# Performance work log

Measured on AMD Instinct MI355X. Metric: run time of the kernel, lower is better.

The kernel has to match this reference:

```python
import jax, jax.numpy as jnp
import numpy as np

IGNORE = 5
N_CLASS = 5
MAX_VIEWS = 2048
MAX_VIEWS_BG = 4096


def setup_inputs() -> dict:
    key = jax.random.key(0)
    ks = jax.random.split(key, 8)
    B, C, H, W = 8, 512, 128, 128
    HF, WF = 1024, 1024
    feats = jax.random.normal(ks[0], (B, C, H, W), dtype=jnp.float32)
    labels = jax.random.uniform(ks[1], (B, HF, WF, N_CLASS), dtype=jnp.float32)
    predicts = jax.random.randint(ks[2], (B, H, W), 0, N_CLASS).astype(jnp.int32)
    s = 0.02
    w1 = jax.random.normal(ks[3], (512, 512), jnp.float32) * s
    b1 = jnp.zeros((512,), jnp.float32)
    w2 = jax.random.normal(ks[4], (256, 512), jnp.float32) * s
    b2 = jnp.zeros((256,), jnp.float32)
    w3 = jax.random.normal(ks[5], (256, 256), jnp.float32) * s
    b3 = jnp.zeros((256,), jnp.float32)
    return dict(feats=feats, labels=labels, predicts=predicts,
                w1=w1, b1=b1, w2=w2, b2=b2, w3=w3, b3=b3)


def _leaky(x):
    return jnp.where(x >= 0, x, 0.2 * x)


def _proj_head(x, w1, b1, w2, b2, w3, b3):
    # Linear -> LeakyReLU(0.2) -> Linear -> LeakyReLU(0.2) -> Linear, then L2-normalize (dim=1)
    h = _leaky(x @ w1.T + b1)
    h = _leaky(h @ w2.T + b2)
    h = h @ w3.T + b3
    nrm = jnp.maximum(jnp.linalg.norm(h, axis=1, keepdims=True), 1e-12)
    return h / nrm


def _sample_class(y_hat, y, feats0, c, mv):
    """Stratified hard/easy pixel selection for class c, padded to static size mv.
    Deterministic take-first-k replaces torch.randperm for reproducibility."""
    N = y_hat.shape[0]
    hard = (y_hat == c) & (y != c)
    easy = (y_hat == c) & (y == c)
    nh = hard.sum().astype(jnp.int32)
    ne = easy.sum().astype(jnp.int32)
    cnt = nh + ne
    valid = (cnt > 1).astype(jnp.int32)   # classes with <=1 pixel are skipped in the original
    n_sel = jnp.minimum(cnt, mv) * valid
    both = (2 * nh >= n_sel) & (2 * ne >= n_sel)
    hk = jnp.where(both, n_sel // 2,
                   jnp.where(2 * nh >= n_sel, n_sel - ne, nh))
    ek = n_sel - hk
    idx = jnp.arange(N, dtype=jnp.int32)
    hsel = hard & ((jnp.cumsum(hard) - 1) < hk)   # first hk hard pixels
    esel = easy & ((jnp.cumsum(easy) - 1) < ek)   # first ek easy pixels
    # stream-compaction: hard first, then easy, then padding
    sort_key = jnp.where(hsel, idx, jnp.where(esel, idx + N, 2 * N))
    order = jnp.argsort(sort_key)[:mv]            # static slice of size mv
    row_ok = jnp.arange(mv) < n_sel
    X = feats0[order] * row_ok[:, None]           # zero-pad invalid rows
    yc = jnp.where(row_ok, c, IGNORE)
    return X, yc.astype(jnp.int32)


def reference(feats, labels, predicts, w1, b1, w2, b2, w3, b3):
    B, C, H, W = feats.shape
    lab = jnp.argmax(labels, axis=-1)             # [B, HF, WF]
    sh, sw = lab.shape[1] // H, lab.shape[2] // W
    lab_ds = lab[:, ::sh, ::sw]                   # nearest-neighbor downsample (integer factor)
    # original _hard_anchor_sampling returns inside the batch loop -> only image 0 contributes
    y_hat = lab_ds[0].reshape(-1).astype(jnp.int32)
    y = predicts[0].reshape(-1).astype(jnp.int32)
    feats0 = feats[0].transpose(1, 2, 0).reshape(H * W, C)  # NHWC flatten
    Xs, ys = [], []
    for c in range(N_CLASS):                      # static small class loop
        mv = MAX_VIEWS_BG if c == 0 else MAX_VIEWS
        Xc, yc = _sample_class(y_hat, y, feats0, c, mv)
        Xs.append(Xc)
        ys.append(yc)
    X_ = jnp.concatenate(Xs, axis=0)              # [MV_bg + 4*MV, 512]
    y_ = jnp.concatenate(ys, axis=0)
    anchors = _proj_head(X_, w1, b1, w2, b2, w3, b3)
    return anchors, y_
```

## Files before the change

kernel.cpp:

```cpp
#include <hip/hip_runtime.h>

#define HW 16384
#define IGN 5
#define ROWS_TOTAL 12288
#define ANCH_ELEMS (ROWS_TOTAL * 256)

typedef __bf16 bf16x8 __attribute__((ext_vector_type(8)));
typedef float f32x4 __attribute__((ext_vector_type(4)));
typedef unsigned long long ull;

#define GLDS16(g, l)                                                                     \
    __builtin_amdgcn_global_load_lds((__attribute__((address_space(1))) const void*)(g), \
                                     (__attribute__((address_space(3))) void*)(l), 16, 0, 0)

__device__ __forceinline__ int swz_off(int row, int chunk) {
    return row * 64 + ((chunk ^ (row & 7)) * 8);
}

__global__ void prep_kernel(const float* __restrict__ labels, const int* __restrict__ predicts,
                            int* __restrict__ y_hat, ull* __restrict__ maskH,
                            ull* __restrict__ maskE, int* __restrict__ fwd) {
    int p = blockIdx.x * 256 + threadIdx.x;
    int pr = p >> 7, pc = p & 127;
    const float* lp = labels + ((size_t)(pr * 8) * 1024 + (size_t)(pc * 8)) * 5;
    float best = lp[0];
    int bi = 0;
#pragma unroll
    for (int c = 1; c < 5; ++c) {
        float v = lp[c];
        if (v > best) { best = v; bi = c; }
    }
    y_hat[p] = bi;
    if (p < ROWS_TOTAL) fwd[p] = -1;
    int yy = predicts[p];
    int chunk = p >> 6;
    int lane = threadIdx.x & 63;
#pragma unroll
    for (int c = 0; c < 5; ++c) {
        ull mh = __ballot(bi == c && yy != c);
        ull me = __ballot(bi == c && yy == c);
        if (lane == 0) {
            maskH[c * 256 + chunk] = mh;
            maskE[c * 256 + chunk] = me;
        }
    }
}

__global__ void scan_kernel(const ull* __restrict__ maskH, const ull* __restrict__ maskE,
                            int* __restrict__ baseH, int* __restrict__ baseE,
                            int* __restrict__ nsel, int* __restrict__ hkA,
                            int* __restrict__ ekA) {
    int c = threadIdx.x >> 6;
    int lane = threadIdx.x & 63;
    if (c >= 5) return;
    int ph[4], pe[4];
    int sh = 0, se = 0;
#pragma unroll
    for (int k = 0; k < 4; ++k) {
        int ch = lane * 4 + k;
        ph[k] = sh;
        sh += __popcll(maskH[c * 256 + ch]);
        pe[k] = se;
        se += __popcll(maskE[c * 256 + ch]);
    }
    int incH = sh, incE = se;
#pragma unroll
    for (int d = 1; d < 64; d <<= 1) {
        int t = __shfl_up(incH, d);
        if (lane >= d) incH += t;
        t = __shfl_up(incE, d);
        if (lane >= d) incE += t;
    }
    int exH = incH - sh, exE = incE - se;
#pragma unroll
    for (int k = 0; k < 4; ++k) {
        baseH[c * 256 + lane * 4 + k] = exH + ph[k];
        baseE[c * 256 + lane * 4 + k] = exE + pe[k];
    }
    int nh = __shfl(incH, 63), ne = __shfl(incE, 63);
    if (lane == 0) {
        int mv = (c == 0) ? 4096 : 2048;
        int cnt = nh + ne;
        int n_sel = (cnt > 1) ? ((cnt < mv) ? cnt : mv) : 0;
        int hk;
        if ((2 * nh >= n_sel) && (2 * ne >= n_sel)) hk = n_sel >> 1;
        else if (2 * nh >= n_sel) hk = n_sel - ne;
        else hk = nh;
        nsel[c] = n_sel;
        hkA[c] = hk;
        ekA[c] = n_sel - hk;
    }
}

__global__ void write_inv_kernel(const int* __restrict__ y_hat,
                                 const ull* __restrict__ maskH, const ull* __restrict__ maskE,
                                 const int* __restrict__ baseH, const int* __restrict__ baseE,
                                 const int* __restrict__ hkA, const int* __restrict__ ekA,
                                 const int* __restrict__ nsel, int* __restrict__ fwd,
                                 float* __restrict__ out) {
    int p = blockIdx.x * 256 + threadIdx.x;
    int chunk = p >> 6;
    int lane = threadIdx.x & 63;
    int c = y_hat[p];
    ull mh = maskH[c * 256 + chunk];
    ull me = maskE[c * 256 + chunk];
    ull below = (1ull << lane) - 1ull;
    int cls_base = (c == 0) ? 0 : 4096 + (c - 1) * 2048;
    int res = -1;
    if ((mh >> lane) & 1ull) {
        int pos = baseH[c * 256 + chunk] + __popcll(mh & below);
        if (pos < hkA[c]) res = cls_base + pos;
    } else if ((me >> lane) & 1ull) {
        int pos = baseE[c * 256 + chunk] + __popcll(me & below);
        if (pos < ekA[c]) res = cls_base + hkA[c] + pos;
    }
    if (res >= 0) fwd[res] = p;
    if (p < ROWS_TOTAL) {
        int cc, rin;
        if (p < 4096) { cc = 0; rin = p; }
        else { cc = 1 + ((p - 4096) >> 11); rin = (p - 4096) & 2047; }
        out[ANCH_ELEMS + p] = (float)(rin < nsel[cc] ? cc : IGN);
    }
}

__global__ void conv_x_kernel(const float* __restrict__ F, __bf16* __restrict__ Xb) {
    __shared__ float t[32 * 33];
    int pb = blockIdx.x * 32, chb = blockIdx.y * 32;
    int tid = threadIdx.x;
    int il = tid & 31;
    int grp = tid >> 5;
#pragma unroll
    for (int it = 0; it < 4; ++it) {
        int ch = grp + it * 8;
        t[il * 33 + ch] = F[(size_t)(chb + ch) * HW + pb + il];
    }
    __syncthreads();
#pragma unroll
    for (int it = 0; it < 4; ++it) {
        int p = grp + it * 8;
        Xb[(size_t)(pb + p) * 512 + chb + il] = (__bf16)t[p * 33 + il];
    }
}

__global__ void conv_w_kernel(const float* __restrict__ w1, const float* __restrict__ w2,
                              const float* __restrict__ w3, __bf16* __restrict__ w1b,
                              __bf16* __restrict__ w2b, __bf16* __restrict__ w3b) {
    int i = blockIdx.x * 256 + threadIdx.x;
    if (i < 262144) w1b[i] = (__bf16)w1[i];
    else if (i < 393216) w2b[i - 262144] = (__bf16)w2[i - 262144];
    else if (i < 458752) w3b[i - 393216] = (__bf16)w3[i - 393216];
}

__global__ __launch_bounds__(256) void gemm_bt(const __bf16* __restrict__ A,
                                               const int* __restrict__ fwd,
                                               const __bf16* __restrict__ Bw,
                                               const float* __restrict__ bias,
                                               __bf16* __restrict__ C, int N, int K,
                                               int leaky) {
    const int BK = 64;
    __shared__ __bf16 As[64 * 64];
    __shared__ __bf16 Bs[128 * 64];
    int tid = threadIdx.x;
    int lane = tid & 63;
    int wave_base = tid & 0xC0;
    int wave = tid >> 6;
    int wm = (wave >> 1) * 32, wn = (wave & 1) * 64;
    int mb = blockIdx.y * 64, nb = blockIdx.x * 128;
    int l15 = lane & 15, quad = lane >> 4;

    const __bf16* srcA[2];
    const __bf16* srcB[4];
#pragma unroll
    for (int r = 0; r < 2; ++r) {
        int cc = tid + r * 256;
        int row = cc >> 3, ch = cc & 7;
        int g = mb + row;
        int pix = fwd ? fwd[g] : g;
        if (pix < 0) pix = 0;
        srcA[r] = A + (size_t)pix * K + ((ch ^ (row & 7)) * 8);
    }
#pragma unroll
    for (int r = 0; r < 4; ++r) {
        int cc = tid + r * 256;
        int row = cc >> 3, ch = cc & 7;
        srcB[r] = Bw + (size_t)(nb + row) * K + ((ch ^ (row & 7)) * 8);
    }

    f32x4 acc[2][4] = {};

    for (int kt = 0; kt < K; kt += BK) {
#pragma unroll
        for (int r = 0; r < 2; ++r)
            GLDS16(srcA[r] + kt, As + (size_t)(r * 256 + wave_base) * 8);
#pragma unroll
        for (int r = 0; r < 4; ++r)
            GLDS16(srcB[r] + kt, Bs + (size_t)(r * 256 + wave_base) * 8);
        __syncthreads();
#pragma unroll
        for (int kk = 0; kk < 2; ++kk) {
            bf16x8 af[2], bq[4];
#pragma unroll
            for (int i = 0; i < 2; ++i)
                af[i] = *(const bf16x8*)(As + swz_off(wm + i * 16 + l15, quad + kk * 4));
#pragma unroll
            for (int j = 0; j < 4; ++j)
                bq[j] = *(const bf16x8*)(Bs + swz_off(wn + j * 16 + l15, quad + kk * 4));
#pragma unroll
            for (int i = 0; i < 2; ++i)
#pragma unroll
                for (int j = 0; j < 4; ++j)
                    acc[i][j] = __builtin_amdgcn_mfma_f32_16x16x32_bf16(af[i], bq[j], acc[i][j], 0, 0, 0);
        }
        __syncthreads();
    }

#pragma unroll
    for (int i = 0; i < 2; ++i) {
#pragma unroll
        for (int j = 0; j < 4; ++j) {
            int col = nb + wn + j * 16 + l15;
            float bv = bias[col];
#pragma unroll
            for (int r = 0; r < 4; ++r) {
                int row = mb + wm + i * 16 + quad * 4 + r;
                float v = acc[i][j][r] + bv;
                if (leaky) v = (v >= 0.f) ? v : 0.2f * v;
                C[(size_t)row * N + col] = (__bf16)v;
            }
        }
    }
}

__global__ __launch_bounds__(256) void gemm3_norm(const __bf16* __restrict__ A,
                                                  const __bf16* __restrict__ W,
                                                  const float* __restrict__ bias,
                                                  const int* __restrict__ fwd,
                                                  float* __restrict__ out) {
    const int BK = 64, K = 256;
    __shared__ __bf16 As[64 * 64];
    __shared__ __bf16 Bs[256 * 64];
    __shared__ __bf16 lo[64 * 264];
    __shared__ float nrm[64];
    int tid = threadIdx.x;
    int lane = tid & 63, wave = tid >> 6;
    int wave_base = tid & 0xC0;
    int l15 = lane & 15, quad = lane >> 4;
    int mb = blockIdx.x * 64;
    int wn = wave * 64;

    if (tid < 64) nrm[tid] = 0.f;

    const __bf16* srcA[2];
    const __bf16* srcB[8];
#pragma unroll
    for (int r = 0; r < 2; ++r) {
        int cc = tid + r * 256;
        int row = cc >> 3, ch = cc & 7;
        srcA[r] = A + (size_t)(mb + row) * K + ((ch ^ (row & 7)) * 8);
    }
#pragma unroll
    for (int r = 0; r < 8; ++r) {
        int cc = tid + r * 256;
        int row = cc >> 3, ch = cc & 7;
        srcB[r] = W + (size_t)row * K + ((ch ^ (row & 7)) * 8);
    }

    f32x4 acc[4][4] = {};

    for (int kt = 0; kt < K; kt += BK) {
#pragma unroll
        for (int r = 0; r < 2; ++r)
            GLDS16(srcA[r] + kt, As + (size_t)(r * 256 + wave_base) * 8);
#pragma unroll
        for (int r = 0; r < 8; ++r)
            GLDS16(srcB[r] + kt, Bs + (size_t)(r * 256 + wave_base) * 8);
        __syncthreads();
#pragma unroll
        for (int kk = 0; kk < 2; ++kk) {
            bf16x8 af[4], bq[4];
#pragma unroll
            for (int i = 0; i < 4; ++i)
                af[i] = *(const bf16x8*)(As + swz_off(i * 16 + l15, quad + kk * 4));
#pragma unroll
            for (int j = 0; j < 4; ++j)
                bq[j] = *(const bf16x8*)(Bs + swz_off(wn + j * 16 + l15, quad + kk * 4));
#pragma unroll
            for (int i = 0; i < 4; ++i)
#pragma unroll
                for (int j = 0; j < 4; ++j)
                    acc[i][j] = __builtin_amdgcn_mfma_f32_16x16x32_bf16(af[i], bq[j], acc[i][j], 0, 0, 0);
        }
        __syncthreads();
    }

#pragma unroll
    for (int i = 0; i < 4; ++i) {
#pragma unroll
        for (int r = 0; r < 4; ++r) {
            int row = i * 16 + quad * 4 + r;
            float s = 0.f;
#pragma unroll
            for (int j = 0; j < 4; ++j) {
                int col = wn + j * 16 + l15;
                float v = acc[i][j][r] + bias[col];
                lo[row * 264 + col] = (__bf16)v;
                s += v * v;
            }
            atomicAdd(&nrm[row], s);
        }
    }
    __syncthreads();
    if (tid < 64) {
        float f = 1.0f / fmaxf(sqrtf(nrm[tid]), 1e-12f);
        nrm[tid] = (fwd[mb + tid] >= 0) ? f : 0.f;
    }
    __syncthreads();

#pragma unroll 4
    for (int r = 0; r < 64; ++r) {
        out[(size_t)(mb + r) * 256 + tid] = (float)lo[r * 264 + tid] * nrm[r];
    }
}

extern "C" void kernel_launch(void* const* d_in, const int* in_sizes, int n_in,
                              void* d_out, int out_size, void* d_ws, size_t ws_size,
                              hipStream_t stream) {
    const float* feats = (const float*)d_in[0];
    const float* labels = (const float*)d_in[1];
    const int* predicts = (const int*)d_in[2];
    const float* w1 = (const float*)d_in[3];
    const float* b1 = (const float*)d_in[4];
    const float* w2 = (const float*)d_in[5];
    const float* b2 = (const float*)d_in[6];
    const float* w3 = (const float*)d_in[7];
    const float* b3 = (const float*)d_in[8];
    float* out = (float*)d_out;
    char* ws = (char*)d_ws;

    int* y_hat = (int*)(ws + 0);
    int* fwd = (int*)(ws + (64 << 10));
    int* nsel = (int*)(ws + (128 << 10));
    int* hkA = (int*)(ws + (128 << 10) + 64);
    int* ekA = (int*)(ws + (128 << 10) + 128);
    ull* maskH = (ull*)(ws + (136 << 10));
    ull* maskE = (ull*)(ws + (148 << 10));
    int* baseH = (int*)(ws + (160 << 10));
    int* baseE = (int*)(ws + (168 << 10));
    __bf16* w1b = (__bf16*)(ws + (256 << 10));
    __bf16* w2b = (__bf16*)(ws + (768 << 10));
    __bf16* w3b = (__bf16*)(ws + (1024 << 10));
    __bf16* Xb = (__bf16*)(ws + (2ull << 20));
    __bf16* H1 = (__bf16*)(ws + (18ull << 20));
    __bf16* H2 = (__bf16*)(ws + (34ull << 20));

    prep_kernel<<<64, 256, 0, stream>>>(labels, predicts, y_hat, maskH, maskE, fwd);
    scan_kernel<<<1, 320, 0, stream>>>(maskH, maskE, baseH, baseE, nsel, hkA, ekA);
    write_inv_kernel<<<64, 256, 0, stream>>>(y_hat, maskH, maskE, baseH, baseE, hkA, ekA,
                                             nsel, fwd, out);
    conv_x_kernel<<<dim3(512, 16), 256, 0, stream>>>(feats, Xb);
    conv_w_kernel<<<1792, 256, 0, stream>>>(w1, w2, w3, w1b, w2b, w3b);
    gemm_bt<<<dim3(4, 192), 256, 0, stream>>>(Xb, fwd, w1b, b1, H1, 512, 512, 1);
    gemm_bt<<<dim3(2, 192), 256, 0, stream>>>(H1, nullptr, w2b, b2, H2, 256, 512, 1);
    gemm3_norm<<<192, 256, 0, stream>>>(H2, w3b, b3, fwd, out);
}
```

Baseline: 430.8 us.

## Fuse prep/convert kernels and merge GEMM2+GEMM3+normalize into one kernel

Merges label prep, weight conversion and the feature transpose into a single launch, with wider vectorized float4/bf16x8 accesses in the transpose. Fuses the second and third MLP layers plus L2 normalization into one kernel that keeps the H2 tile in LDS, so H2 is never written to global memory. The norm is now reduced with shuffles, and the GEMM1 grid is reordered to iterate M-major. This removes launch overhead and intermediate global traffic. In exchange the fused kernel uses more LDS per block with 32-row tiles, and the W3 load is serialized after GEMM2.

```diff
diff --git a/kernel.cpp b/kernel.cpp
--- a/kernel.cpp
+++ b/kernel.cpp
@@ -17,32 +17,78 @@
     return row * 64 + ((chunk ^ (row & 7)) * 8);
 }
 
-__global__ void prep_kernel(const float* __restrict__ labels, const int* __restrict__ predicts,
-                            int* __restrict__ y_hat, ull* __restrict__ maskH,
-                            ull* __restrict__ maskE, int* __restrict__ fwd) {
-    int p = blockIdx.x * 256 + threadIdx.x;
-    int pr = p >> 7, pc = p & 127;
-    const float* lp = labels + ((size_t)(pr * 8) * 1024 + (size_t)(pc * 8)) * 5;
-    float best = lp[0];
-    int bi = 0;
-#pragma unroll
-    for (int c = 1; c < 5; ++c) {
-        float v = lp[c];
-        if (v > best) { best = v; bi = c; }
-    }
-    y_hat[p] = bi;
-    if (p < ROWS_TOTAL) fwd[p] = -1;
-    int yy = predicts[p];
-    int chunk = p >> 6;
-    int lane = threadIdx.x & 63;
-#pragma unroll
-    for (int c = 0; c < 5; ++c) {
-        ull mh = __ballot(bi == c && yy != c);
-        ull me = __ballot(bi == c && yy == c);
-        if (lane == 0) {
-            maskH[c * 256 + chunk] = mh;
-            maskE[c * 256 + chunk] = me;
-        }
+__global__ void prep_fused(const float* __restrict__ labels, const int* __restrict__ predicts,
+                           int* __restrict__ y_hat, ull* __restrict__ maskH,
+                           ull* __restrict__ maskE, int* __restrict__ fwd,
+                           const float* __restrict__ w1, const float* __restrict__ w2,
+                           const float* __restrict__ w3, __bf16* __restrict__ w1b,
+                           __bf16* __restrict__ w2b, __bf16* __restrict__ w3b,
+                           const float* __restrict__ F, __bf16* __restrict__ Xb) {
+    __shared__ float t[64][68];
+    int bid = blockIdx.x;
+    int tid = threadIdx.x;
+    if (bid < 64) {
+        int p = bid * 256 + tid;
+        int pr = p >> 7, pc = p & 127;
+        const float* lp = labels + ((size_t)(pr * 8) * 1024 + (size_t)(pc * 8)) * 5;
+        float best = lp[0];
+        int bi = 0;
+#pragma unroll
+        for (int c = 1; c < 5; ++c) {
+            float v = lp[c];
+            if (v > best) { best = v; bi = c; }
+        }
+        y_hat[p] = bi;
+        if (p < ROWS_TOTAL) fwd[p] = -1;
+        int yy = predicts[p];
+        int chunk = p >> 6;
+        int lane = tid & 63;
+#pragma unroll
+        for (int c = 0; c < 5; ++c) {
+            ull mh = __ballot(bi == c && yy != c);
+            ull me = __ballot(bi == c && yy == c);
+            if (lane == 0) {
+                maskH[c * 256 + chunk] = mh;
+                maskE[c * 256 + chunk] = me;
+            }
+        }
+    } else if (bid < 512) {
+        int base = ((bid - 64) * 256 + tid) * 4;
+        if (base < 262144) {
+            float4 v = *(const float4*)(w1 + base);
+            w1b[base + 0] = (__bf16)v.x; w1b[base + 1] = (__bf16)v.y;
+            w1b[base + 2] = (__bf16)v.z; w1b[base + 3] = (__bf16)v.w;
+        } else if (base < 393216) {
+            int o = base - 262144;
+            float4 v = *(const float4*)(w2 + o);
+            w2b[o + 0] = (__bf16)v.x; w2b[o + 1] = (__bf16)v.y;
+            w2b[o + 2] = (__bf16)v.z; w2b[o + 3] = (__bf16)v.w;
+        } else {
+            int o = base - 393216;
+            float4 v = *(const float4*)(w3 + o);
+            w3b[o + 0] = (__bf16)v.x; w3b[o + 1] = (__bf16)v.y;
+            w3b[o + 2] = (__bf16)v.z; w3b[o + 3] = (__bf16)v.w;
+        }
+    } else {
+        int cid = bid - 512;
+        int pb = (cid & 255) * 64;
+        int chb = (cid >> 8) * 64;
+        int row = tid >> 2;
+        int seg = tid & 3;
+        const float* src = F + (size_t)(chb + row) * HW + pb + seg * 16;
+#pragma unroll
+        for (int k = 0; k < 4; ++k)
+            *(float4*)&t[row][seg * 16 + k * 4] = *(const float4*)(src + k * 4);
+        __syncthreads();
+        int p = tid >> 2;
+        __bf16* dst = Xb + (size_t)(pb + p) * 512 + chb + seg * 16;
+        bf16x8 o0, o1;
+#pragma unroll
+        for (int j = 0; j < 8; ++j) o0[j] = (__bf16)t[seg * 16 + j][p];
+#pragma unroll
+        for (int j = 0; j < 8; ++j) o1[j] = (__bf16)t[seg * 16 + 8 + j][p];
+        *(bf16x8*)dst = o0;
+        *(bf16x8*)(dst + 8) = o1;
     }
 }
 
@@ -123,34 +169,6 @@
     }
 }
 
-__global__ void conv_x_kernel(const float* __restrict__ F, __bf16* __restrict__ Xb) {
-    __shared__ float t[32 * 33];
-    int pb = blockIdx.x * 32, chb = blockIdx.y * 32;
-    int tid = threadIdx.x;
-    int il = tid & 31;
-    int grp = tid >> 5;
-#pragma unroll
-    for (int it = 0; it < 4; ++it) {
-        int ch = grp + it * 8;
-        t[il * 33 + ch] = F[(size_t)(chb + ch) * HW + pb + il];
-    }
-    __syncthreads();
-#pragma unroll
-    for (int it = 0; it < 4; ++it) {
-        int p = grp + it * 8;
-        Xb[(size_t)(pb + p) * 512 + chb + il] = (__bf16)t[p * 33 + il];
-    }
-}
-
-__global__ void conv_w_kernel(const float* __restrict__ w1, const float* __restrict__ w2,
-                              const float* __restrict__ w3, __bf16* __restrict__ w1b,
-                              __bf16* __restrict__ w2b, __bf16* __restrict__ w3b) {
-    int i = blockIdx.x * 256 + threadIdx.x;
-    if (i < 262144) w1b[i] = (__bf16)w1[i];
-    else if (i < 393216) w2b[i - 262144] = (__bf16)w2[i - 262144];
-    else if (i < 458752) w3b[i - 393216] = (__bf16)w3[i - 393216];
-}
-
 __global__ __launch_bounds__(256) void gemm_bt(const __bf16* __restrict__ A,
                                                const int* __restrict__ fwd,
                                                const __bf16* __restrict__ Bw,
@@ -165,7 +183,7 @@
     int wave_base = tid & 0xC0;
     int wave = tid >> 6;
     int wm = (wave >> 1) * 32, wn = (wave & 1) * 64;
-    int mb = blockIdx.y * 64, nb = blockIdx.x * 128;
+    int mb = blockIdx.x * 64, nb = blockIdx.y * 128;
     int l15 = lane & 15, quad = lane >> 4;
 
     const __bf16* srcA[2];
@@ -231,61 +249,54 @@
     }
 }
 
-__global__ __launch_bounds__(256) void gemm3_norm(const __bf16* __restrict__ A,
-                                                  const __bf16* __restrict__ W,
-                                                  const float* __restrict__ bias,
-                                                  const int* __restrict__ fwd,
-                                                  float* __restrict__ out) {
-    const int BK = 64, K = 256;
-    __shared__ __bf16 As[64 * 64];
-    __shared__ __bf16 Bs[256 * 64];
-    __shared__ __bf16 lo[64 * 264];
-    __shared__ float nrm[64];
+__global__ __launch_bounds__(256) void gemm23_norm(const __bf16* __restrict__ H1,
+                                                   const __bf16* __restrict__ W2b,
+                                                   const float* __restrict__ b2,
+                                                   const __bf16* __restrict__ W3b,
+                                                   const float* __restrict__ b3,
+                                                   const int* __restrict__ fwd,
+                                                   float* __restrict__ out) {
+    __shared__ __bf16 As[32 * 64];
+    __shared__ __bf16 Ws[256 * 64];
+    __shared__ __bf16 H2s[4][32 * 64];
+    __shared__ float nrm[32];
     int tid = threadIdx.x;
     int lane = tid & 63, wave = tid >> 6;
     int wave_base = tid & 0xC0;
     int l15 = lane & 15, quad = lane >> 4;
-    int mb = blockIdx.x * 64;
+    int mb = blockIdx.x * 32;
     int wn = wave * 64;
 
-    if (tid < 64) nrm[tid] = 0.f;
-
-    const __bf16* srcA[2];
-    const __bf16* srcB[8];
-#pragma unroll
-    for (int r = 0; r < 2; ++r) {
-        int cc = tid + r * 256;
-        int row = cc >> 3, ch = cc & 7;
-        srcA[r] = A + (size_t)(mb + row) * K + ((ch ^ (row & 7)) * 8);
-    }
+    if (tid < 32) nrm[tid] = 0.f;
+
+    int rowA = tid >> 3, chA = tid & 7;
+    const __bf16* srcA = H1 + (size_t)(mb + rowA) * 512 + ((chA ^ (rowA & 7)) * 8);
+    const __bf16* srcW2[8];
 #pragma unroll
     for (int r = 0; r < 8; ++r) {
         int cc = tid + r * 256;
         int row = cc >> 3, ch = cc & 7;
-        srcB[r] = W + (size_t)row * K + ((ch ^ (row & 7)) * 8);
-    }
-
-    f32x4 acc[4][4] = {};
-
-    for (int kt = 0; kt < K; kt += BK) {
-#pragma unroll
-        for (int r = 0; r < 2; ++r)
-            GLDS16(srcA[r] + kt, As + (size_t)(r * 256 + wave_base) * 8);
+        srcW2[r] = W2b + (size_t)row * 512 + ((ch ^ (row & 7)) * 8);
+    }
+
+    f32x4 acc[2][4] = {};
+    for (int kt = 0; kt < 512; kt += 64) {
+        GLDS16(srcA + kt, As + (size_t)wave_base * 8);
 #pragma unroll
         for (int r = 0; r < 8; ++r)
-            GLDS16(srcB[r] + kt, Bs + (size_t)(r * 256 + wave_base) * 8);
+            GLDS16(srcW2[r] + kt, Ws + (size_t)(r * 256 + wave_base) * 8);
         __syncthreads();
 #pragma unroll
         for (int kk = 0; kk < 2; ++kk) {
-            bf16x8 af[4], bq[4];
-#pragma unroll
-            for (int i = 0; i < 4; ++i)
+            bf16x8 af[2], bq[4];
+#pragma unroll
+            for (int i = 0; i < 2; ++i)
                 af[i] = *(const bf16x8*)(As + swz_off(i * 16 + l15, quad + kk * 4));
 #pragma unroll
             for (int j = 0; j < 4; ++j)
-                bq[j] = *(const bf16x8*)(Bs + swz_off(wn + j * 16 + l15, quad + kk * 4));
-#pragma unroll
-            for (int i = 0; i < 4; ++i)
+                bq[j] = *(const bf16x8*)(Ws + swz_off(wn + j * 16 + l15, quad + kk * 4));
+#pragma unroll
+            for (int i = 0; i < 2; ++i)
 #pragma unroll
                 for (int j = 0; j < 4; ++j)
                     acc[i][j] = __builtin_amdgcn_mfma_f32_16x16x32_bf16(af[i], bq[j], acc[i][j], 0, 0, 0);
@@ -294,31 +305,104 @@
     }
 
 #pragma unroll
-    for (int i = 0; i < 4; ++i) {
+    for (int i = 0; i < 2; ++i) {
+#pragma unroll
+        for (int j = 0; j < 4; ++j) {
+            int col = wn + j * 16 + l15;
+            float bv = b2[col];
+            int ktb = col >> 6;
+            int chunk = (col >> 3) & 7;
+#pragma unroll
+            for (int r = 0; r < 4; ++r) {
+                int row = i * 16 + quad * 4 + r;
+                float v = acc[i][j][r] + bv;
+                v = (v >= 0.f) ? v : 0.2f * v;
+                H2s[ktb][row * 64 + ((chunk ^ (row & 7)) * 8) + (col & 7)] = (__bf16)v;
+            }
+        }
+    }
+    __syncthreads();
+
+    const __bf16* srcW3[8];
+#pragma unroll
+    for (int r = 0; r < 8; ++r) {
+        int cc = tid + r * 256;
+        int row = cc >> 3, ch = cc & 7;
+        srcW3[r] = W3b + (size_t)row * 256 + ((ch ^ (row & 7)) * 8);
+    }
+    f32x4 acc3[2][4] = {};
+    for (int ktb = 0; ktb < 4; ++ktb) {
+#pragma unroll
+        for (int r = 0; r < 8; ++r)
+            GLDS16(srcW3[r] + ktb * 64, Ws + (size_t)(r * 256 + wave_base) * 8);
+        __syncthreads();
+#pragma unroll
+        for (int kk = 0; kk < 2; ++kk) {
+            bf16x8 af[2], bq[4];
+#pragma unroll
+            for (int i = 0; i < 2; ++i)
+                af[i] = *(const bf16x8*)(&H2s[ktb][0] + swz_off(i * 16 + l15, quad + kk * 4));
+#pragma unroll
+            for (int j = 0; j < 4; ++j)
+                bq[j] = *(const bf16x8*)(Ws + swz_off(wn + j * 16 + l15, quad + kk * 4));
+#pragma unroll
+            for (int i = 0; i < 2; ++i)
+#pragma unroll
+                for (int j = 0; j < 4; ++j)
+                    acc3[i][j] = __builtin_amdgcn_mfma_f32_16x16x32_bf16(af[i], bq[j], acc3[i][j], 0, 0, 0);
+        }
+        __syncthreads();
+    }
+
+    float vs[2][4][4];
+    float ss[2][4];
+#pragma unroll
+    for (int i = 0; i < 2; ++i)
+#pragma unroll
+        for (int r = 0; r < 4; ++r) ss[i][r] = 0.f;
+#pragma unroll
+    for (int i = 0; i < 2; ++i) {
+#pragma unroll
+        for (int j = 0; j < 4; ++j) {
+            int col = wn + j * 16 + l15;
+            float bv = b3[col];
+#pragma unroll
+            for (int r = 0; r < 4; ++r) {
+                float v = acc3[i][j][r] + bv;
+                vs[i][j][r] = v;
+                ss[i][r] += v * v;
+            }
+        }
+    }
+#pragma unroll
+    for (int i = 0; i < 2; ++i) {
 #pragma unroll
         for (int r = 0; r < 4; ++r) {
-            int row = i * 16 + quad * 4 + r;
-            float s = 0.f;
-#pragma unroll
-            for (int j = 0; j < 4; ++j) {
-                int col = wn + j * 16 + l15;
-                float v = acc[i][j][r] + bias[col];
-                lo[row * 264 + col] = (__bf16)v;
-                s += v * v;
-            }
-            atomicAdd(&nrm[row], s);
+            float s = ss[i][r];
+            s += __shfl_xor(s, 1);
+            s += __shfl_xor(s, 2);
+            s += __shfl_xor(s, 4);
+            s += __shfl_xor(s, 8);
+            if (l15 == 0) atomicAdd(&nrm[i * 16 + quad * 4 + r], s);
         }
     }
     __syncthreads();
-    if (tid < 64) {
+    if (tid < 32) {
         float f = 1.0f / fmaxf(sqrtf(nrm[tid]), 1e-12f);
         nrm[tid] = (fwd[mb + tid] >= 0) ? f : 0.f;
     }
     __syncthreads();
-
-#pragma unroll 4
-    for (int r = 0; r < 64; ++r) {
-        out[(size_t)(mb + r) * 256 + tid] = (float)lo[r * 264 + tid] * nrm[r];
+#pragma unroll
+    for (int i = 0; i < 2; ++i) {
+#pragma unroll
+        for (int j = 0; j < 4; ++j) {
+            int col = wn + j * 16 + l15;
+#pragma unroll
+            for (int r = 0; r < 4; ++r) {
+                int row = i * 16 + quad * 4 + r;
+                out[(size_t)(mb + row) * 256 + col] = vs[i][j][r] * nrm[row];
+            }
+        }
     }
 }
 
@@ -351,15 +435,12 @@
     __bf16* w3b = (__bf16*)(ws + (1024 << 10));
     __bf16* Xb = (__bf16*)(ws + (2ull << 20));
     __bf16* H1 = (__bf16*)(ws + (18ull << 20));
-    __bf16* H2 = (__bf16*)(ws + (34ull << 20));
-
-    prep_kernel<<<64, 256, 0, stream>>>(labels, predicts, y_hat, maskH, maskE, fwd);
+
+    prep_fused<<<2560, 256, 0, stream>>>(labels, predicts, y_hat, maskH, maskE, fwd,
+                                         w1, w2, w3, w1b, w2b, w3b, feats, Xb);
     scan_kernel<<<1, 320, 0, stream>>>(maskH, maskE, baseH, baseE, nsel, hkA, ekA);
     write_inv_kernel<<<64, 256, 0, stream>>>(y_hat, maskH, maskE, baseH, baseE, hkA, ekA,
                                              nsel, fwd, out);
-    conv_x_kernel<<<dim3(512, 16), 256, 0, stream>>>(feats, Xb);
-    conv_w_kernel<<<1792, 256, 0, stream>>>(w1, w2, w3, w1b, w2b, w3b);
-    gemm_bt<<<dim3(4, 192), 256, 0, stream>>>(Xb, fwd, w1b, b1, H1, 512, 512, 1);
-    gemm_bt<<<dim3(2, 192), 256, 0, stream>>>(H1, nullptr, w2b, b2, H2, 256, 512, 1);
-    gemm3_norm<<<192, 256, 0, stream>>>(H2, w3b, b3, fwd, out);
-}
+    gemm_bt<<<dim3(192, 4), 256, 0, stream>>>(Xb, fwd, w1b, b1, H1, 512, 512, 1);
+    gemm23_norm<<<384, 256, 0, stream>>>(H1, w2b, b2, w3b, b3, fwd, out);
+}
```

New measurement: 412.5 us. 1.04x faster.
